# Performance work log

Measured on AMD Instinct MI355X. Metric: run time of the kernel, lower is better.

The kernel has to match this reference:

```python
import jax, jax.numpy as jnp
import numpy as np

N = 50000
E = 800000
IN_DIM = 128
OUT_DIM = 128
EDGE_DIM = 3
H = 4
HD = OUT_DIM // H  # 32
SCALE = HD ** -0.5


def setup_inputs() -> dict:
    key = jax.random.key(0)
    ks = jax.random.split(key, 10)
    x = jax.random.normal(ks[0], (N, IN_DIM), dtype=jnp.float32)
    edge_index = jax.random.randint(ks[1], (2, E), 0, N, dtype=jnp.int64)
    edge_attr = jax.random.normal(ks[2], (E, EDGE_DIM), dtype=jnp.float32)
    s = 1.0 / np.sqrt(IN_DIM)
    Wq = jax.random.normal(ks[3], (IN_DIM, H * HD), dtype=jnp.float32) * s
    Wk = jax.random.normal(ks[4], (IN_DIM, H * HD), dtype=jnp.float32) * s
    Wv = jax.random.normal(ks[5], (IN_DIM, H * HD), dtype=jnp.float32) * s
    We = jax.random.normal(ks[6], (EDGE_DIM, H), dtype=jnp.float32) * (1.0 / np.sqrt(EDGE_DIM))
    Wo = jax.random.normal(ks[7], (H * HD, OUT_DIM), dtype=jnp.float32) * (1.0 / np.sqrt(H * HD))
    bo = jnp.zeros((OUT_DIM,), dtype=jnp.float32)
    Wm = jax.random.normal(ks[8], (IN_DIM + OUT_DIM, OUT_DIM), dtype=jnp.float32) * (1.0 / np.sqrt(IN_DIM + OUT_DIM))
    bm = jnp.zeros((OUT_DIM,), dtype=jnp.float32)
    return {"x": x, "edge_index": edge_index, "edge_attr": edge_attr,
            "Wq": Wq, "Wk": Wk, "Wv": Wv, "We": We, "Wo": Wo, "bo": bo,
            "Wm": Wm, "bm": bm}


def reference(x, edge_index, edge_attr, Wq, Wk, Wv, We, Wo, bo, Wm, bm):
    n = x.shape[0]
    src = edge_index[0]
    dst = edge_index[1]
    Q = (x @ Wq).reshape(n, H, HD)
    K = (x @ Wk).reshape(n, H, HD)
    V = (x @ Wv).reshape(n, H, HD)
    edge_bias = edge_attr @ We                                  # [E, H]
    attn = jnp.sum(Q[dst] * K[src], axis=-1) * SCALE + edge_bias  # [E, H]
    attn = jnp.where(attn >= 0, attn, 0.2 * attn)               # leaky_relu(0.2)
    # NOTE: original uses a single GLOBAL max over all edges/heads for stability
    attn_exp = jnp.exp(attn - jnp.max(attn))
    attn_sum = jax.ops.segment_sum(attn_exp, dst, num_segments=n)  # [N, H]
    attn_norm = attn_exp / jnp.maximum(attn_sum[dst], 1e-12)
    # dropout disabled (eval mode)
    weighted_V = V[src] * attn_norm[:, :, None]                 # [E, H, HD]
    agg = jax.ops.segment_sum(weighted_V, dst, num_segments=n)  # [N, H, HD]
    agg = agg.reshape(n, H * HD) @ Wo + bo                      # [N, OUT]
    h = jnp.concatenate([x, agg], axis=1) @ Wm + bm
    return jax.nn.relu(h)
```

## Files before the change

kernel.cpp:

```cpp
#include <hip/hip_runtime.h>
#include <hip/hip_bf16.h>
#include <math.h>

#define NN 50000
#define NE 800000
#define DIM 128
#define NH 4
#define HD 32
#define ATTN_SCALE 0.17677669529663687f
#define MTILE 64
#define GEMM_BLOCKS 782
#define NBK 782
#define PTS 2048
#define HBLKS 104

#define K1_QKV_BASE 104
#define K1_WXB_BASE 296
#define K1_GRID     361
#define K3_PART_N     391
#define K3_PACKO_BASE 391
#define K3_XCVT_BASE  519
#define K3_GRID       6769
#define K4_CSR_N 782
#define K4_GRID  1564

typedef unsigned int uint;
typedef unsigned short ushort;
typedef __attribute__((ext_vector_type(8))) short short8;
typedef __attribute__((ext_vector_type(4))) float f32x4;

__device__ inline ushort f2bf(float f) {
    __hip_bfloat16 h = __float2bfloat16(f);
    return *(ushort*)&h;
}
__device__ inline float bflo(uint u) { return __uint_as_float(u << 16); }
__device__ inline float bfhi(uint u) { return __uint_as_float(u & 0xffff0000u); }
__device__ inline float bf2f(ushort u) { return __uint_as_float((uint)u << 16); }

__global__ __launch_bounds__(256) void k1_kernel(
    const int* __restrict__ dst, int* __restrict__ bkt_cnt,
    const float* __restrict__ Wq, const float* __restrict__ Wk,
    const float* __restrict__ Wv, short* __restrict__ BpQKV,
    const float* __restrict__ Wo, const float* __restrict__ Wm,
    const float* __restrict__ bo, const float* __restrict__ bm,
    float* __restrict__ Wx, float* __restrict__ bprime)
{
    const int bid = blockIdx.x;
    const int tid = threadIdx.x;

    if (bid < HBLKS) {
        __shared__ int c[NBK];
        for (int l = tid; l < NBK; l += 256) c[l] = 0;
        __syncthreads();
        for (int e = bid * 256 + tid; e < NE; e += HBLKS * 256)
            atomicAdd(&c[dst[e] >> 6], 1);
        __syncthreads();
        for (int l = tid; l < NBK; l += 256)
            if (c[l]) atomicAdd(&bkt_cnt[l], c[l]);
    } else if (bid < K1_WXB_BASE) {
        const int idx = (bid - K1_QKV_BASE) * 256 + tid;
        const int j = idx & 7, lane = (idx >> 3) & 63;
        const int rest = idx >> 9;
        const int nt = rest % 24, kc = rest / 24;
        const int k = kc * 32 + (lane >> 4) * 8 + j;
        const int n = nt * 16 + (lane & 15);
        const float* W = (n < 128) ? Wq : (n < 256 ? Wk : Wv);
        BpQKV[idx] = (short)f2bf(W[k * 128 + (n & 127)]);
    } else {
        const int r = (bid - K1_WXB_BASE) * 2 + (tid >> 7);
        const int j = tid & 127;
        if (r < 128) {
            float acc = 0.f;
            for (int t = 0; t < 128; ++t)
                acc = fmaf(Wo[r * 128 + t], Wm[(128 + t) * 128 + j], acc);
            Wx[r * 128 + j] = acc;
        } else if (r == 128) {
            float acc = bm[j];
            for (int t = 0; t < 128; ++t)
                acc = fmaf(bo[t], Wm[(128 + t) * 128 + j], acc);
            bprime[j] = acc;
        }
    }
}

__global__ __launch_bounds__(256) void bkt_scan_kernel(
    const int* __restrict__ bkt_cnt,
    int* __restrict__ bkt_base, int* __restrict__ bkt_cursor,
    int* __restrict__ rowptr)
{
    __shared__ int part[256];
    const int tid = threadIdx.x;
    const int b0 = tid * 4;
    int v0 = 0, v1 = 0, v2 = 0, v3 = 0;
    if (b0 + 0 < NBK) v0 = bkt_cnt[b0 + 0];
    if (b0 + 1 < NBK) v1 = bkt_cnt[b0 + 1];
    if (b0 + 2 < NBK) v2 = bkt_cnt[b0 + 2];
    if (b0 + 3 < NBK) v3 = bkt_cnt[b0 + 3];
    const int s = v0 + v1 + v2 + v3;
    part[tid] = s;
    __syncthreads();
    for (int off = 1; off < 256; off <<= 1) {
        const int y = (tid >= off) ? part[tid - off] : 0;
        __syncthreads();
        part[tid] += y;
        __syncthreads();
    }
    const int ex = part[tid] - s;
    const int r0 = ex, r1 = ex + v0, r2 = ex + v0 + v1, r3 = ex + v0 + v1 + v2;
    if (b0 + 0 < NBK) { bkt_base[b0 + 0] = r0; bkt_cursor[b0 + 0] = r0; }
    if (b0 + 1 < NBK) { bkt_base[b0 + 1] = r1; bkt_cursor[b0 + 1] = r1; }
    if (b0 + 2 < NBK) { bkt_base[b0 + 2] = r2; bkt_cursor[b0 + 2] = r2; }
    if (b0 + 3 < NBK) { bkt_base[b0 + 3] = r3; bkt_cursor[b0 + 3] = r3; }
    if (tid == 255) bkt_base[NBK] = part[255];
    if (tid == 0)   rowptr[NN] = NE;
}

__global__ __launch_bounds__(256) void k3_kernel(
    const int* __restrict__ src, const int* __restrict__ dst,
    const float* __restrict__ edge_attr, const float* __restrict__ We,
    int* __restrict__ bkt_cursor,
    uint* __restrict__ ppack, uint2* __restrict__ pebp,
    const float* __restrict__ Wm, const float* __restrict__ Wx,
    short* __restrict__ BpOut,
    const float* __restrict__ x, ushort* __restrict__ xb)
{
    const int bid = blockIdx.x;
    const int tid = threadIdx.x;

    if (bid < K3_PART_N) {
        __shared__ int cnt[NBK], rbase[NBK], cnt2[NBK];
        for (int l = tid; l < NBK; l += 256) cnt[l] = 0;
        __syncthreads();
        const int e0 = bid * PTS;
        #pragma unroll
        for (int it = 0; it < 8; ++it) {
            const int e = e0 + it * 256 + tid;
            if (e < NE) atomicAdd(&cnt[dst[e] >> 6], 1);
        }
        __syncthreads();
        for (int l = tid; l < NBK; l += 256) {
            const int c = cnt[l];
            rbase[l] = c ? atomicAdd(&bkt_cursor[l], c) : 0;
            cnt2[l] = 0;
        }
        __syncthreads();
        #pragma unroll
        for (int it = 0; it < 8; ++it) {
            const int e = e0 + it * 256 + tid;
            if (e < NE) {
                const int d = dst[e];
                const int b = d >> 6;
                const int r = atomicAdd(&cnt2[b], 1);
                const int pos = rbase[b] + r;
                ppack[pos] = (uint)src[e] | ((uint)(d & 63) << 16);
                const float a0 = edge_attr[e * 3 + 0];
                const float a1 = edge_attr[e * 3 + 1];
                const float a2 = edge_attr[e * 3 + 2];
                const float b0 = a0 * We[0] + a1 * We[4] + a2 * We[8];
                const float b1 = a0 * We[1] + a1 * We[5] + a2 * We[9];
                const float b2 = a0 * We[2] + a1 * We[6] + a2 * We[10];
                const float b3 = a0 * We[3] + a1 * We[7] + a2 * We[11];
                uint2 ep;
                ep.x = (uint)f2bf(b0) | ((uint)f2bf(b1) << 16);
                ep.y = (uint)f2bf(b2) | ((uint)f2bf(b3) << 16);
                pebp[pos] = ep;
            }
        }
    } else if (bid < K3_XCVT_BASE) {
        const int idx = (bid - K3_PACKO_BASE) * 256 + tid;
        const int j = idx & 7, lane = (idx >> 3) & 63;
        const int rest = idx >> 9;
        const int nt = rest & 7, kc = rest >> 3;
        const int k = kc * 32 + (lane >> 4) * 8 + j;
        const int n = nt * 16 + (lane & 15);
        const float v = (k < 128) ? Wm[k * 128 + n] : Wx[(k - 128) * 128 + n];
        BpOut[idx] = (short)f2bf(v);
    } else {
        const int i = (bid - K3_XCVT_BASE) * 256 + tid;
        const float4 v = ((const float4*)x)[i];
        ushort4 o;
        o.x = f2bf(v.x); o.y = f2bf(v.y); o.z = f2bf(v.z); o.w = f2bf(v.w);
        ((ushort4*)xb)[i] = o;
    }
}

__global__ __launch_bounds__(256) void k4_kernel(
    const int* __restrict__ bkt_base,
    const uint* __restrict__ ppack, const uint2* __restrict__ pebp,
    int* __restrict__ rowptr,
    ushort* __restrict__ srcp, uint2* __restrict__ ebq,
    const ushort* __restrict__ xb, const short* __restrict__ BpQKV,
    ushort* __restrict__ Qb, ushort* __restrict__ KVb)
{
    const int bid = blockIdx.x;
    const int tid = threadIdx.x;

    if (bid < K4_CSR_N) {
        __shared__ int cnt[64];
        __shared__ int pre[64];
        const int base = bkt_base[bid];
        const int n = bkt_base[bid + 1] - base;
        const int node0 = bid << 6;

        if (tid < 64) cnt[tid] = 0;
        __syncthreads();
        for (int i = base + tid; i < base + n; i += 256)
            atomicAdd(&cnt[ppack[i] >> 16], 1);
        __syncthreads();

        if (tid < 64) {
            const int c = cnt[tid];
            int xsc = c;
            #pragma unroll
            for (int off = 1; off < 64; off <<= 1) {
                const int y = __shfl_up(xsc, off);
                if (tid >= off) xsc += y;
            }
            const int ex = base + xsc - c;
            pre[tid] = ex;
            const int g = node0 + tid;
            if (g < NN) rowptr[g] = ex;
        }
        __syncthreads();

        for (int i = base + tid; i < base + n; i += 256) {
            const uint v = ppack[i];
            const int pos = atomicAdd(&pre[v >> 16], 1);
            srcp[pos] = (ushort)(v & 0xFFFFu);
            ebq[pos] = pebp[i];
        }
    } else {
        const int qb = bid - K4_CSR_N;
        const int wave = tid >> 6;
        const int lane = tid & 63;
        const int m = lane & 15, quad = lane >> 4;
        const int row0w = qb * MTILE + wave * 16;
        const int arow = row0w + m;
        const bool rowok = arow < NN;

        short8 a[4];
        #pragma unroll
        for (int kc = 0; kc < 4; ++kc)
            a[kc] = rowok ? *(const short8*)(xb + (size_t)arow * 128 + kc * 32 + quad * 8)
                          : (short8)(0);

        const int NT = 24;
        for (int nt = 0; nt < NT; nt += 2) {
            f32x4 acc0 = {0.f, 0.f, 0.f, 0.f}, acc1 = {0.f, 0.f, 0.f, 0.f};
            #pragma unroll
            for (int kc = 0; kc < 4; ++kc) {
                const short8 b0 = *(const short8*)(BpQKV + ((size_t)(kc * NT + nt) * 64 + lane) * 8);
                const short8 b1 = *(const short8*)(BpQKV + ((size_t)(kc * NT + nt + 1) * 64 + lane) * 8);
                acc0 = __builtin_amdgcn_mfma_f32_16x16x32_bf16(a[kc], b0, acc0, 0, 0, 0);
                acc1 = __builtin_amdgcn_mfma_f32_16x16x32_bf16(a[kc], b1, acc1, 0, 0, 0);
            }
            #pragma unroll
            for (int t = 0; t < 2; ++t) {
                const f32x4 acc = t ? acc1 : acc0;
                const int c = (nt + t) * 16 + m;
                #pragma unroll
                for (int g = 0; g < 4; ++g) {
                    const int r = row0w + quad * 4 + g;
                    if (r < NN) {
                        if (c < 128) Qb[(size_t)r * 128 + c] = f2bf(acc[g]);
                        else        KVb[(size_t)r * 256 + (c - 128)] = f2bf(acc[g]);
                    }
                }
            }
        }
    }
}

__global__ __launch_bounds__(256) void out_mfma_kernel(
    const ushort* __restrict__ xb, const ushort* __restrict__ aggb,
    const short* __restrict__ Bp, const float* __restrict__ bprime,
    float* __restrict__ out)
{
    const int wave = threadIdx.x >> 6;
    const int lane = threadIdx.x & 63;
    const int m = lane & 15, quad = lane >> 4;
    const int row0w = blockIdx.x * MTILE + wave * 16;
    const int arow = row0w + m;
    const bool rowok = arow < NN;

    short8 a[8];
    #pragma unroll
    for (int kc = 0; kc < 4; ++kc)
        a[kc] = rowok ? *(const short8*)(xb + (size_t)arow * 128 + kc * 32 + quad * 8)
                      : (short8)(0);
    #pragma unroll
    for (int kc = 0; kc < 4; ++kc)
        a[4 + kc] = rowok ? *(const short8*)(aggb + (size_t)arow * 128 + kc * 32 + quad * 8)
                          : (short8)(0);

    const int NT = 8;
    for (int nt = 0; nt < NT; nt += 2) {
        f32x4 acc0 = {0.f, 0.f, 0.f, 0.f}, acc1 = {0.f, 0.f, 0.f, 0.f};
        #pragma unroll
        for (int kc = 0; kc < 8; ++kc) {
            const short8 b0 = *(const short8*)(Bp + ((size_t)(kc * NT + nt) * 64 + lane) * 8);
            const short8 b1 = *(const short8*)(Bp + ((size_t)(kc * NT + nt + 1) * 64 + lane) * 8);
            acc0 = __builtin_amdgcn_mfma_f32_16x16x32_bf16(a[kc], b0, acc0, 0, 0, 0);
            acc1 = __builtin_amdgcn_mfma_f32_16x16x32_bf16(a[kc], b1, acc1, 0, 0, 0);
        }
        #pragma unroll
        for (int t = 0; t < 2; ++t) {
            const f32x4 acc = t ? acc1 : acc0;
            const int c = (nt + t) * 16 + m;
            const float bb = bprime[c];
            #pragma unroll
            for (int g = 0; g < 4; ++g) {
                const int r = row0w + quad * 4 + g;
                if (r < NN) out[(size_t)r * 128 + c] = fmaxf(acc[g] + bb, 0.f);
            }
        }
    }
}

__global__ __launch_bounds__(256) void attn_agg_kernel(
    const ushort* __restrict__ Qb, const ushort* __restrict__ KVb,
    const int* __restrict__ rowptr, const ushort* __restrict__ srcp,
    const ushort* __restrict__ ebb, ushort* __restrict__ aggb)
{
    const int tid = threadIdx.x;
    const int d = blockIdx.x * 4 + (tid >> 6);
    const int lane = tid & 63;
    const int g = lane >> 4;
    const int t = lane & 15;
    const int h = t >> 2;
    const int begin = rowptr[d];
    const int end   = rowptr[d + 1];

    const uint4 uq = *(const uint4*)(Qb + (size_t)d * DIM + 8 * t);
    const float q0 = bflo(uq.x), q1 = bfhi(uq.x);
    const float q2 = bflo(uq.y), q3 = bfhi(uq.y);
    const float q4 = bflo(uq.z), q5 = bfhi(uq.z);
    const float q6 = bflo(uq.w), q7 = bfhi(uq.w);

    float ss = 0.f;
    float a0 = 0.f, a1 = 0.f, a2 = 0.f, a3 = 0.f;
    float a4 = 0.f, a5 = 0.f, a6 = 0.f, a7 = 0.f;

    if (begin < end) {
        int ec = begin + g;
        if (ec >= end) ec = end - 1;
        int s    = (int)srcp[ec];
        float eb = bf2f(ebb[ec * 4 + h]);

        for (int p = begin; p < end; p += 4) {
            const bool ok = (p + g) < end;
            const int pn = p + 4;
            int sn = s; float ebn = eb;
            if (pn < end) {
                int en = pn + g;
                if (en >= end) en = end - 1;
                sn  = (int)srcp[en];
                ebn = bf2f(ebb[en * 4 + h]);
            }

            const ushort* kv = KVb + (size_t)s * 256 + 8 * t;
            const uint4 uk = *(const uint4*)(kv);
            const uint4 uv = *(const uint4*)(kv + 128);

            float da = q0 * bflo(uk.x);
            float db = q1 * bfhi(uk.x);
            da = fmaf(q2, bflo(uk.y), da);
            db = fmaf(q3, bfhi(uk.y), db);
            da = fmaf(q4, bflo(uk.z), da);
            db = fmaf(q5, bfhi(uk.z), db);
            da = fmaf(q6, bflo(uk.w), da);
            db = fmaf(q7, bfhi(uk.w), db);
            float part = da + db;
            part += __shfl_xor(part, 1);
            part += __shfl_xor(part, 2);

            float a = fmaf(part, ATTN_SCALE, eb);
            a = (a >= 0.f) ? a : 0.2f * a;
            float w = ok ? __expf(a) : 0.f;

            ss += w;
            a0 = fmaf(w, bflo(uv.x), a0);
            a1 = fmaf(w, bfhi(uv.x), a1);
            a2 = fmaf(w, bflo(uv.y), a2);
            a3 = fmaf(w, bfhi(uv.y), a3);
            a4 = fmaf(w, bflo(uv.z), a4);
            a5 = fmaf(w, bfhi(uv.z), a5);
            a6 = fmaf(w, bflo(uv.w), a6);
            a7 = fmaf(w, bfhi(uv.w), a7);

            s = sn; eb = ebn;
        }
    }

    ss += __shfl_xor(ss, 16);
    ss += __shfl_xor(ss, 32);
    a0 += __shfl_xor(a0, 16); a0 += __shfl_xor(a0, 32);
    a1 += __shfl_xor(a1, 16); a1 += __shfl_xor(a1, 32);
    a2 += __shfl_xor(a2, 16); a2 += __shfl_xor(a2, 32);
    a3 += __shfl_xor(a3, 16); a3 += __shfl_xor(a3, 32);
    a4 += __shfl_xor(a4, 16); a4 += __shfl_xor(a4, 32);
    a5 += __shfl_xor(a5, 16); a5 += __shfl_xor(a5, 32);
    a6 += __shfl_xor(a6, 16); a6 += __shfl_xor(a6, 32);
    a7 += __shfl_xor(a7, 16); a7 += __shfl_xor(a7, 32);

    if (g == 0) {
        const float inv = 1.f / fmaxf(ss, 1e-12f);
        uint4 o;
        o.x = (uint)f2bf(a0 * inv) | ((uint)f2bf(a1 * inv) << 16);
        o.y = (uint)f2bf(a2 * inv) | ((uint)f2bf(a3 * inv) << 16);
        o.z = (uint)f2bf(a4 * inv) | ((uint)f2bf(a5 * inv) << 16);
        o.w = (uint)f2bf(a6 * inv) | ((uint)f2bf(a7 * inv) << 16);
        *(uint4*)(aggb + (size_t)d * DIM + 8 * t) = o;
    }
}

extern "C" void kernel_launch(void* const* d_in, const int* in_sizes, int n_in,
                              void* d_out, int out_size, void* d_ws, size_t ws_size,
                              hipStream_t stream)
{
    const float* x         = (const float*)d_in[0];
    const int*   edge_idx  = (const int*)d_in[1];
    const float* edge_attr = (const float*)d_in[2];
    const float* Wq        = (const float*)d_in[3];
    const float* Wk        = (const float*)d_in[4];
    const float* Wv        = (const float*)d_in[5];
    const float* We        = (const float*)d_in[6];
    const float* Wo        = (const float*)d_in[7];
    const float* bo        = (const float*)d_in[8];
    const float* Wm        = (const float*)d_in[9];
    const float* bm        = (const float*)d_in[10];
    float* out = (float*)d_out;

    const int* src = edge_idx;
    const int* dst = edge_idx + NE;

    ushort* xb   = (ushort*)d_ws;
    ushort* Qb   = xb + (size_t)NN * DIM;
    ushort* KVb  = Qb + (size_t)NN * DIM;
    ushort* aggb = KVb + (size_t)NN * 2 * DIM;
    uint*  ppack = (uint*)(aggb + (size_t)NN * DIM);
    uint2* pebp  = (uint2*)(ppack + NE);
    uint2* ebq   = pebp + NE;
    ushort* srcp = (ushort*)(ebq + NE);
    float* Wx    = (float*)(srcp + NE);
    float* bprime= Wx + 16384;
    short* BpQKV = (short*)(bprime + 128);
    short* BpOut = BpQKV + 49152;
    int*   rowptr= (int*)(BpOut + 32768);
    int*   bkt_cnt    = rowptr + 50048;
    int*   bkt_base   = bkt_cnt + 800;
    int*   bkt_cursor = bkt_base + 800;

    hipMemsetAsync(bkt_cnt, 0, NBK * sizeof(int), stream);

    k1_kernel<<<K1_GRID, 256, 0, stream>>>(
        dst, bkt_cnt, Wq, Wk, Wv, BpQKV, Wo, Wm, bo, bm, Wx, bprime);

    bkt_scan_kernel<<<1, 256, 0, stream>>>(bkt_cnt, bkt_base, bkt_cursor, rowptr);

    k3_kernel<<<K3_GRID, 256, 0, stream>>>(
        src, dst, edge_attr, We, bkt_cursor, ppack, pebp, Wm, Wx, BpOut, x, xb);

    k4_kernel<<<K4_GRID, 256, 0, stream>>>(
        bkt_base, ppack, pebp, rowptr, srcp, ebq, xb, BpQKV, Qb, KVb);

    attn_agg_kernel<<<NN / 4, 256, 0, stream>>>(Qb, KVb, rowptr, srcp,
                                                (const ushort*)ebq, aggb);

    out_mfma_kernel<<<GEMM_BLOCKS, 256, 0, stream>>>(xb, aggb, BpOut, bprime, out);
}
```

Before: 245.4 us.

## Build CSR with per-node atomics, fuse QKV GEMM and drop bf16 x copy

Replaces the two-level bucket sort (bucket histogram, bucket scatter, per-bucket CSR pass) with a per-node histogram, a single-block scan over all nodes, and direct atomic scatter into 16-byte per-edge records holding src and the edge bias. The QKV GEMM moves into the scatter kernel, which removes one launch. Both GEMMs now read fp32 x and convert it to bf16 in registers, so the separate conversion pass is gone. In exchange there is heavy global atomic contention on per-node cursors, a serial single-block scan over 50k nodes, wider edge records, and non-deterministic edge order within a node.

Result: slower. 405.1 us (+65.1%).

```diff
diff --git a/kernel.cpp b/kernel.cpp
--- a/kernel.cpp
+++ b/kernel.cpp
@@ -10,19 +10,16 @@
 #define ATTN_SCALE 0.17677669529663687f
 #define MTILE 64
 #define GEMM_BLOCKS 782
-#define NBK 782
 #define PTS 2048
-#define HBLKS 104
-
-#define K1_QKV_BASE 104
-#define K1_WXB_BASE 296
-#define K1_GRID     361
-#define K3_PART_N     391
+
+#define K1_HIST_N   782
+#define K1_QKV_BASE 782
+#define K1_WXB_BASE 974
+#define K1_GRID     1039
+#define K3_SCAT_N     391
 #define K3_PACKO_BASE 391
-#define K3_XCVT_BASE  519
-#define K3_GRID       6769
-#define K4_CSR_N 782
-#define K4_GRID  1564
+#define K3_GEMM_BASE  519
+#define K3_GRID       1301
 
 typedef unsigned int uint;
 typedef unsigned short ushort;
@@ -35,10 +32,9 @@
 }
 __device__ inline float bflo(uint u) { return __uint_as_float(u << 16); }
 __device__ inline float bfhi(uint u) { return __uint_as_float(u & 0xffff0000u); }
-__device__ inline float bf2f(ushort u) { return __uint_as_float((uint)u << 16); }
 
 __global__ __launch_bounds__(256) void k1_kernel(
-    const int* __restrict__ dst, int* __restrict__ bkt_cnt,
+    const int* __restrict__ dst, int* __restrict__ nodecnt,
     const float* __restrict__ Wq, const float* __restrict__ Wk,
     const float* __restrict__ Wv, short* __restrict__ BpQKV,
     const float* __restrict__ Wo, const float* __restrict__ Wm,
@@ -48,15 +44,13 @@
     const int bid = blockIdx.x;
     const int tid = threadIdx.x;
 
-    if (bid < HBLKS) {
-        __shared__ int c[NBK];
-        for (int l = tid; l < NBK; l += 256) c[l] = 0;
-        __syncthreads();
-        for (int e = bid * 256 + tid; e < NE; e += HBLKS * 256)
-            atomicAdd(&c[dst[e] >> 6], 1);
-        __syncthreads();
-        for (int l = tid; l < NBK; l += 256)
-            if (c[l]) atomicAdd(&bkt_cnt[l], c[l]);
+    if (bid < K1_HIST_N) {
+        const int e0 = bid * 1024;
+        #pragma unroll
+        for (int it = 0; it < 4; ++it) {
+            const int e = e0 + it * 256 + tid;
+            if (e < NE) atomicAdd(&nodecnt[dst[e]], 1);
+        }
     } else if (bid < K1_WXB_BASE) {
         const int idx = (bid - K1_QKV_BASE) * 256 + tid;
         const int j = idx & 7, lane = (idx >> 3) & 63;
@@ -83,20 +77,18 @@
     }
 }
 
-__global__ __launch_bounds__(256) void bkt_scan_kernel(
-    const int* __restrict__ bkt_cnt,
-    int* __restrict__ bkt_base, int* __restrict__ bkt_cursor,
-    int* __restrict__ rowptr)
+__global__ __launch_bounds__(256) void scan_kernel(
+    const int* __restrict__ nodecnt,
+    int* __restrict__ rowptr, int* __restrict__ cursor)
 {
     __shared__ int part[256];
     const int tid = threadIdx.x;
-    const int b0 = tid * 4;
-    int v0 = 0, v1 = 0, v2 = 0, v3 = 0;
-    if (b0 + 0 < NBK) v0 = bkt_cnt[b0 + 0];
-    if (b0 + 1 < NBK) v1 = bkt_cnt[b0 + 1];
-    if (b0 + 2 < NBK) v2 = bkt_cnt[b0 + 2];
-    if (b0 + 3 < NBK) v3 = bkt_cnt[b0 + 3];
-    const int s = v0 + v1 + v2 + v3;
+    const int i0 = tid * 196;
+    int s = 0;
+    for (int k = 0; k < 196; ++k) {
+        const int i = i0 + k;
+        if (i < NN) s += nodecnt[i];
+    }
     part[tid] = s;
     __syncthreads();
     for (int off = 1; off < 256; off <<= 1) {
@@ -105,68 +97,58 @@
         part[tid] += y;
         __syncthreads();
     }
-    const int ex = part[tid] - s;
-    const int r0 = ex, r1 = ex + v0, r2 = ex + v0 + v1, r3 = ex + v0 + v1 + v2;
-    if (b0 + 0 < NBK) { bkt_base[b0 + 0] = r0; bkt_cursor[b0 + 0] = r0; }
-    if (b0 + 1 < NBK) { bkt_base[b0 + 1] = r1; bkt_cursor[b0 + 1] = r1; }
-    if (b0 + 2 < NBK) { bkt_base[b0 + 2] = r2; bkt_cursor[b0 + 2] = r2; }
-    if (b0 + 3 < NBK) { bkt_base[b0 + 3] = r3; bkt_cursor[b0 + 3] = r3; }
-    if (tid == 255) bkt_base[NBK] = part[255];
-    if (tid == 0)   rowptr[NN] = NE;
+    int run = part[tid] - s;
+    for (int k = 0; k < 196; ++k) {
+        const int i = i0 + k;
+        if (i < NN) {
+            rowptr[i] = run;
+            cursor[i] = run;
+            run += nodecnt[i];
+        }
+    }
+    if (tid == 255) rowptr[NN] = run;
 }
 
 __global__ __launch_bounds__(256) void k3_kernel(
     const int* __restrict__ src, const int* __restrict__ dst,
     const float* __restrict__ edge_attr, const float* __restrict__ We,
-    int* __restrict__ bkt_cursor,
-    uint* __restrict__ ppack, uint2* __restrict__ pebp,
+    int* __restrict__ cursor, uint4* __restrict__ edata,
     const float* __restrict__ Wm, const float* __restrict__ Wx,
     short* __restrict__ BpOut,
-    const float* __restrict__ x, ushort* __restrict__ xb)
+    const float* __restrict__ x, const short* __restrict__ BpQKV,
+    ushort* __restrict__ Qb, ushort* __restrict__ KVb)
 {
     const int bid = blockIdx.x;
     const int tid = threadIdx.x;
 
-    if (bid < K3_PART_N) {
-        __shared__ int cnt[NBK], rbase[NBK], cnt2[NBK];
-        for (int l = tid; l < NBK; l += 256) cnt[l] = 0;
-        __syncthreads();
+    if (bid < K3_SCAT_N) {
+        float we[12];
+        #pragma unroll
+        for (int i = 0; i < 12; ++i) we[i] = We[i];
         const int e0 = bid * PTS;
-        #pragma unroll
-        for (int it = 0; it < 8; ++it) {
-            const int e = e0 + it * 256 + tid;
-            if (e < NE) atomicAdd(&cnt[dst[e] >> 6], 1);
-        }
-        __syncthreads();
-        for (int l = tid; l < NBK; l += 256) {
-            const int c = cnt[l];
-            rbase[l] = c ? atomicAdd(&bkt_cursor[l], c) : 0;
-            cnt2[l] = 0;
-        }
-        __syncthreads();
         #pragma unroll
         for (int it = 0; it < 8; ++it) {
             const int e = e0 + it * 256 + tid;
             if (e < NE) {
                 const int d = dst[e];
-                const int b = d >> 6;
-                const int r = atomicAdd(&cnt2[b], 1);
-                const int pos = rbase[b] + r;
-                ppack[pos] = (uint)src[e] | ((uint)(d & 63) << 16);
+                const int s = src[e];
+                const int pos = atomicAdd(&cursor[d], 1);
                 const float a0 = edge_attr[e * 3 + 0];
                 const float a1 = edge_attr[e * 3 + 1];
                 const float a2 = edge_attr[e * 3 + 2];
-                const float b0 = a0 * We[0] + a1 * We[4] + a2 * We[8];
-                const float b1 = a0 * We[1] + a1 * We[5] + a2 * We[9];
-                const float b2 = a0 * We[2] + a1 * We[6] + a2 * We[10];
-                const float b3 = a0 * We[3] + a1 * We[7] + a2 * We[11];
-                uint2 ep;
-                ep.x = (uint)f2bf(b0) | ((uint)f2bf(b1) << 16);
-                ep.y = (uint)f2bf(b2) | ((uint)f2bf(b3) << 16);
-                pebp[pos] = ep;
-            }
-        }
-    } else if (bid < K3_XCVT_BASE) {
+                const float b0 = a0 * we[0] + a1 * we[4] + a2 * we[8];
+                const float b1 = a0 * we[1] + a1 * we[5] + a2 * we[9];
+                const float b2 = a0 * we[2] + a1 * we[6] + a2 * we[10];
+                const float b3 = a0 * we[3] + a1 * we[7] + a2 * we[11];
+                uint4 rec;
+                rec.x = (uint)s;
+                rec.y = (uint)f2bf(b0) | ((uint)f2bf(b1) << 16);
+                rec.z = (uint)f2bf(b2) | ((uint)f2bf(b3) << 16);
+                rec.w = 0u;
+                edata[pos] = rec;
+            }
+        }
+    } else if (bid < K3_GEMM_BASE) {
         const int idx = (bid - K3_PACKO_BASE) * 256 + tid;
         const int j = idx & 7, lane = (idx >> 3) & 63;
         const int rest = idx >> 9;
@@ -176,61 +158,7 @@
         const float v = (k < 128) ? Wm[k * 128 + n] : Wx[(k - 128) * 128 + n];
         BpOut[idx] = (short)f2bf(v);
     } else {
-        const int i = (bid - K3_XCVT_BASE) * 256 + tid;
-        const float4 v = ((const float4*)x)[i];
-        ushort4 o;
-        o.x = f2bf(v.x); o.y = f2bf(v.y); o.z = f2bf(v.z); o.w = f2bf(v.w);
-        ((ushort4*)xb)[i] = o;
-    }
-}
-
-__global__ __launch_bounds__(256) void k4_kernel(
-    const int* __restrict__ bkt_base,
-    const uint* __restrict__ ppack, const uint2* __restrict__ pebp,
-    int* __restrict__ rowptr,
-    ushort* __restrict__ srcp, uint2* __restrict__ ebq,
-    const ushort* __restrict__ xb, const short* __restrict__ BpQKV,
-    ushort* __restrict__ Qb, ushort* __restrict__ KVb)
-{
-    const int bid = blockIdx.x;
-    const int tid = threadIdx.x;
-
-    if (bid < K4_CSR_N) {
-        __shared__ int cnt[64];
-        __shared__ int pre[64];
-        const int base = bkt_base[bid];
-        const int n = bkt_base[bid + 1] - base;
-        const int node0 = bid << 6;
-
-        if (tid < 64) cnt[tid] = 0;
-        __syncthreads();
-        for (int i = base + tid; i < base + n; i += 256)
-            atomicAdd(&cnt[ppack[i] >> 16], 1);
-        __syncthreads();
-
-        if (tid < 64) {
-            const int c = cnt[tid];
-            int xsc = c;
-            #pragma unroll
-            for (int off = 1; off < 64; off <<= 1) {
-                const int y = __shfl_up(xsc, off);
-                if (tid >= off) xsc += y;
-            }
-            const int ex = base + xsc - c;
-            pre[tid] = ex;
-            const int g = node0 + tid;
-            if (g < NN) rowptr[g] = ex;
-        }
-        __syncthreads();
-
-        for (int i = base + tid; i < base + n; i += 256) {
-            const uint v = ppack[i];
-            const int pos = atomicAdd(&pre[v >> 16], 1);
-            srcp[pos] = (ushort)(v & 0xFFFFu);
-            ebq[pos] = pebp[i];
-        }
-    } else {
-        const int qb = bid - K4_CSR_N;
+        const int qb = bid - K3_GEMM_BASE;
         const int wave = tid >> 6;
         const int lane = tid & 63;
         const int m = lane & 15, quad = lane >> 4;
@@ -239,10 +167,23 @@
         const bool rowok = arow < NN;
 
         short8 a[4];
-        #pragma unroll
-        for (int kc = 0; kc < 4; ++kc)
-            a[kc] = rowok ? *(const short8*)(xb + (size_t)arow * 128 + kc * 32 + quad * 8)
-                          : (short8)(0);
+        if (rowok) {
+            const float* xr = x + (size_t)arow * 128;
+            #pragma unroll
+            for (int kc = 0; kc < 4; ++kc) {
+                const float4 f0 = *(const float4*)(xr + kc * 32 + quad * 8);
+                const float4 f1 = *(const float4*)(xr + kc * 32 + quad * 8 + 4);
+                short8 v;
+                v[0] = (short)f2bf(f0.x); v[1] = (short)f2bf(f0.y);
+                v[2] = (short)f2bf(f0.z); v[3] = (short)f2bf(f0.w);
+                v[4] = (short)f2bf(f1.x); v[5] = (short)f2bf(f1.y);
+                v[6] = (short)f2bf(f1.z); v[7] = (short)f2bf(f1.w);
+                a[kc] = v;
+            }
+        } else {
+            #pragma unroll
+            for (int kc = 0; kc < 4; ++kc) a[kc] = (short8)(0);
+        }
 
         const int NT = 24;
         for (int nt = 0; nt < NT; nt += 2) {
@@ -272,7 +213,7 @@
 }
 
 __global__ __launch_bounds__(256) void out_mfma_kernel(
-    const ushort* __restrict__ xb, const ushort* __restrict__ aggb,
+    const float* __restrict__ x, const ushort* __restrict__ aggb,
     const short* __restrict__ Bp, const float* __restrict__ bprime,
     float* __restrict__ out)
 {
@@ -284,14 +225,26 @@
     const bool rowok = arow < NN;
 
     short8 a[8];
-    #pragma unroll
-    for (int kc = 0; kc < 4; ++kc)
-        a[kc] = rowok ? *(const short8*)(xb + (size_t)arow * 128 + kc * 32 + quad * 8)
-                      : (short8)(0);
-    #pragma unroll
-    for (int kc = 0; kc < 4; ++kc)
-        a[4 + kc] = rowok ? *(const short8*)(aggb + (size_t)arow * 128 + kc * 32 + quad * 8)
-                          : (short8)(0);
+    if (rowok) {
+        const float* xr = x + (size_t)arow * 128;
+        #pragma unroll
+        for (int kc = 0; kc < 4; ++kc) {
+            const float4 f0 = *(const float4*)(xr + kc * 32 + quad * 8);
+            const float4 f1 = *(const float4*)(xr + kc * 32 + quad * 8 + 4);
+            short8 v;
+            v[0] = (short)f2bf(f0.x); v[1] = (short)f2bf(f0.y);
+            v[2] = (short)f2bf(f0.z); v[3] = (short)f2bf(f0.w);
+            v[4] = (short)f2bf(f1.x); v[5] = (short)f2bf(f1.y);
+            v[6] = (short)f2bf(f1.z); v[7] = (short)f2bf(f1.w);
+            a[kc] = v;
+        }
+        #pragma unroll
+        for (int kc = 0; kc < 4; ++kc)
+            a[4 + kc] = *(const short8*)(aggb + (size_t)arow * 128 + kc * 32 + quad * 8);
+    } else {
+        #pragma unroll
+        for (int kc = 0; kc < 8; ++kc) a[kc] = (short8)(0);
+    }
 
     const int NT = 8;
     for (int nt = 0; nt < NT; nt += 2) {
@@ -319,8 +272,8 @@
 
 __global__ __launch_bounds__(256) void attn_agg_kernel(
     const ushort* __restrict__ Qb, const ushort* __restrict__ KVb,
-    const int* __restrict__ rowptr, const ushort* __restrict__ srcp,
-    const ushort* __restrict__ ebb, ushort* __restrict__ aggb)
+    const int* __restrict__ rowptr, const uint4* __restrict__ edata,
+    ushort* __restrict__ aggb)
 {
     const int tid = threadIdx.x;
     const int d = blockIdx.x * 4 + (tid >> 6);
@@ -344,19 +297,21 @@
     if (begin < end) {
         int ec = begin + g;
         if (ec >= end) ec = end - 1;
-        int s    = (int)srcp[ec];
-        float eb = bf2f(ebb[ec * 4 + h]);
+        uint4 rec = edata[ec];
 
         for (int p = begin; p < end; p += 4) {
             const bool ok = (p + g) < end;
             const int pn = p + 4;
-            int sn = s; float ebn = eb;
+            uint4 recn = rec;
             if (pn < end) {
                 int en = pn + g;
                 if (en >= end) en = end - 1;
-                sn  = (int)srcp[en];
-                ebn = bf2f(ebb[en * 4 + h]);
-            }
+                recn = edata[en];
+            }
+
+            const int s = (int)rec.x;
+            const uint wrd = (h & 2) ? rec.z : rec.y;
+            const float eb = (h & 1) ? bfhi(wrd) : bflo(wrd);
 
             const ushort* kv = KVb + (size_t)s * 256 + 8 * t;
             const uint4 uk = *(const uint4*)(kv);
@@ -376,7 +331,7 @@
 
             float a = fmaf(part, ATTN_SCALE, eb);
             a = (a >= 0.f) ? a : 0.2f * a;
-            float w = ok ? __expf(a) : 0.f;
+            const float w = ok ? __expf(a) : 0.f;
 
             ss += w;
             a0 = fmaf(w, bflo(uv.x), a0);
@@ -388,7 +343,7 @@
             a6 = fmaf(w, bflo(uv.w), a6);
             a7 = fmaf(w, bfhi(uv.w), a7);
 
-            s = sn; eb = ebn;
+            rec = recn;
         }
     }
 
@@ -434,38 +389,30 @@
     const int* src = edge_idx;
     const int* dst = edge_idx + NE;
 
-    ushort* xb   = (ushort*)d_ws;
-    ushort* Qb   = xb + (size_t)NN * DIM;
+    ushort* Qb   = (ushort*)d_ws;
     ushort* KVb  = Qb + (size_t)NN * DIM;
     ushort* aggb = KVb + (size_t)NN * 2 * DIM;
-    uint*  ppack = (uint*)(aggb + (size_t)NN * DIM);
-    uint2* pebp  = (uint2*)(ppack + NE);
-    uint2* ebq   = pebp + NE;
-    ushort* srcp = (ushort*)(ebq + NE);
-    float* Wx    = (float*)(srcp + NE);
+    uint4* edata = (uint4*)(aggb + (size_t)NN * DIM);
+    float* Wx    = (float*)(edata + NE);
     float* bprime= Wx + 16384;
     short* BpQKV = (short*)(bprime + 128);
     short* BpOut = BpQKV + 49152;
     int*   rowptr= (int*)(BpOut + 32768);
-    int*   bkt_cnt    = rowptr + 50048;
-    int*   bkt_base   = bkt_cnt + 800;
-    int*   bkt_cursor = bkt_base + 800;
-
-    hipMemsetAsync(bkt_cnt, 0, NBK * sizeof(int), stream);
+    int*   cursor = rowptr + 50048;
+    int*   nodecnt= cursor + 50048;
+
+    hipMemsetAsync(nodecnt, 0, 50048 * sizeof(int), stream);
 
     k1_kernel<<<K1_GRID, 256, 0, stream>>>(
-        dst, bkt_cnt, Wq, Wk, Wv, BpQKV, Wo, Wm, bo, bm, Wx, bprime);
-
-    bkt_scan_kernel<<<1, 256, 0, stream>>>(bkt_cnt, bkt_base, bkt_cursor, rowptr);
+        dst, nodecnt, Wq, Wk, Wv, BpQKV, Wo, Wm, bo, bm, Wx, bprime);
+
+    scan_kernel<<<1, 256, 0, stream>>>(nodecnt, rowptr, cursor);
 
     k3_kernel<<<K3_GRID, 256, 0, stream>>>(
-        src, dst, edge_attr, We, bkt_cursor, ppack, pebp, Wm, Wx, BpOut, x, xb);
-
-    k4_kernel<<<K4_GRID, 256, 0, stream>>>(
-        bkt_base, ppack, pebp, rowptr, srcp, ebq, xb, BpQKV, Qb, KVb);
-
-    attn_agg_kernel<<<NN / 4, 256, 0, stream>>>(Qb, KVb, rowptr, srcp,
-                                                (const ushort*)ebq, aggb);
-
-    out_mfma_kernel<<<GEMM_BLOCKS, 256, 0, stream>>>(xb, aggb, BpOut, bprime, out);
-}
+        src, dst, edge_attr, We, cursor, edata, Wm, Wx, BpOut,
+        x, BpQKV, Qb, KVb);
+
+    attn_agg_kernel<<<NN / 4, 256, 0, stream>>>(Qb, KVb, rowptr, edata, aggb);
+
+    out_mfma_kernel<<<GEMM_BLOCKS, 256, 0, stream>>>(x, aggb, BpOut, bprime, out);
+}
```
